# Performance work log

Measured on AMD Instinct MI355X. Metric: run time of the kernel, lower is better.

## Reference

```python
import jax, jax.numpy as jnp
import numpy as np

B, C_IN, H, W = 2, 256, 64, 64
D, NH, WS = 128, 8, 8          # embed_dim, num_heads, window_size
N_PTS = 8192
CAP = 256                      # max tokens per window (64 pixels + points, padded)
ODE_STEPS = 4                  # fixed-step RK4 approximating dopri5 on t in [0,1]


def setup_inputs() -> dict:
    key = jax.random.key(0)
    ks = jax.random.split(key, 16)
    p = lambda k, shape, fan: (jax.random.normal(k, shape, jnp.float32) / np.float32(np.sqrt(fan)))
    return {
        "in_image_feat": jax.random.normal(ks[0], (B, C_IN, H, W), jnp.float32),
        "pts_uv": jax.random.randint(ks[1], (N_PTS, 3), 0, 64),
        "pts_feat": jax.random.normal(ks[2], (N_PTS, D), jnp.float32),
        "conv_in_w": p(ks[3], (D, C_IN), C_IN),         # conv256_128 (1x1)
        "conv_in_b": jnp.zeros((D,), jnp.float32),
        "qkv_w": p(ks[4], (3 * D, D), D),               # sptr attn qkv
        "qkv_b": jnp.zeros((3 * D,), jnp.float32),
        "attnproj_w": p(ks[5], (D, D), D),              # sptr attn out proj
        "attnproj_b": jnp.zeros((D,), jnp.float32),
        "ode_w": p(ks[6], (D, D), D),                   # outimagefc128_128_ode
        "ode_b": jnp.zeros((D,), jnp.float32),
        "conv_out_w": p(ks[7], (C_IN, D), D),           # conv128_256 (1x1)
        "conv_out_b": jnp.zeros((C_IN,), jnp.float32),
    }


def _windowed_attention(feat, wid, NW, qkv_w, qkv_b, proj_w, proj_b):
    """Var-length windowed MHSA (sptr.VarLengthMultiheadSA) via pad-to-CAP."""
    T, d = feat.shape
    hd = d // NH
    order = jnp.argsort(wid)                      # stable sort by window id
    wid_s, feat_s = wid[order], feat[order]
    counts = jax.ops.segment_sum(jnp.ones_like(wid), wid, num_segments=NW)
    starts = jnp.cumsum(counts) - counts
    rank = jnp.arange(T) - starts[wid_s]          # within-window position
    valid = rank < CAP
    wid_w = jnp.where(valid, wid_s, NW)           # overflow -> dummy window
    rank_w = jnp.where(valid, rank, 0)
    buf = jnp.zeros((NW + 1, CAP, d), feat.dtype).at[wid_w, rank_w].set(feat_s)
    msk = jnp.zeros((NW + 1, CAP), bool).at[wid_w, rank_w].set(valid)
    qkv = buf @ qkv_w.T + qkv_b                   # [NW+1, CAP, 3d]
    q, k, v = (t.reshape(NW + 1, CAP, NH, hd) for t in jnp.split(qkv, 3, axis=-1))
    scores = jnp.einsum('wqhd,wkhd->whqk', q, k) / np.float32(np.sqrt(hd))
    scores = jnp.where(msk[:, None, None, :], scores, jnp.float32(-1e9))
    attn = jax.nn.softmax(scores, axis=-1)
    o = jnp.einsum('whqk,wkhd->wqhd', attn, v).reshape(NW + 1, CAP, d)
    o = o @ proj_w.T + proj_b
    out_s = jnp.where(valid[:, None], o[wid_w, rank_w], feat_s)
    return jnp.zeros_like(out_s).at[order].set(out_s)  # unsort


def reference(in_image_feat, pts_uv, pts_feat, conv_in_w, conv_in_b,
              qkv_w, qkv_b, attnproj_w, attnproj_b,
              ode_w, ode_b, conv_out_w, conv_out_b):
    b, c, h, w = in_image_feat.shape
    d = conv_in_w.shape[0]
    # 1x1 conv 256->128
    x = jnp.einsum('bchw,ec->bhwe', in_image_feat, conv_in_w) + conv_in_b
    pix_feat = x.reshape(b * h * w, d)
    # pixel uv grid (convert_image_to_uv): flatten order (b, h, w); u=w idx, v=h idx
    vv, uu = jnp.meshgrid(jnp.arange(h), jnp.arange(w), indexing='ij')
    pix_b = jnp.repeat(jnp.arange(b), h * w)
    pix_u = jnp.tile(uu.reshape(-1), b)
    pix_v = jnp.tile(vv.reshape(-1), b)
    # projected point uv (convert_pts_to_uv result, made in-range)
    pts_b = pts_uv[:, 0] % b
    pts_u = pts_uv[:, 1] % w
    pts_v = pts_uv[:, 2] % h
    tok_b = jnp.concatenate([pix_b, pts_b])
    tok_u = jnp.concatenate([pix_u, pts_u])
    tok_v = jnp.concatenate([pix_v, pts_v])
    feat = jnp.concatenate([pix_feat, pts_feat], axis=0)
    nwx, nwy = w // WS, h // WS
    wid = (tok_b * nwy + tok_v // WS) * nwx + tok_u // WS
    NW = b * nwx * nwy
    out = _windowed_attention(feat, wid, NW, qkv_w, qkv_b, attnproj_w, attnproj_b)
    img = out[: b * h * w]
    # fcode branch: odeint(ODEFunc(Linear), t=[0,1]) ~ fixed-step RK4, + residual
    f = lambda y: jax.nn.relu(y @ ode_w.T + ode_b)
    dt = jnp.float32(1.0 / ODE_STEPS)
    y = img
    for _ in range(ODE_STEPS):
        k1 = f(y); k2 = f(y + 0.5 * dt * k1); k3 = f(y + 0.5 * dt * k2); k4 = f(y + dt * k3)
        y = y + (dt / 6.0) * (k1 + 2.0 * k2 + 2.0 * k3 + k4)
    img = y + img
    # 1x1 conv 128->256 back to image layout
    img = img.reshape(b, h, w, d)
    return jnp.einsum('bhwd,cd->bchw', img, conv_out_w) + conv_out_b[None, :, None, None]
```

## Files before the change

### kernel.cpp

```cpp
#include <hip/hip_runtime.h>

typedef short bf16x8 __attribute__((ext_vector_type(8)));
typedef float f32x4 __attribute__((ext_vector_type(4)));

__device__ __forceinline__ float b2f(unsigned short s) {
    union { float f; unsigned u; } x; x.u = ((unsigned)s) << 16; return x.f;
}
__device__ __forceinline__ unsigned short f2b(float f) {
    unsigned u = __float_as_uint(f);
    unsigned r = (u + 0x7fffu + ((u >> 16) & 1u)) >> 16;
    return (unsigned short)r;
}

__global__ __launch_bounds__(256) void cast_k(const float* __restrict__ ciw,
                                              const float* __restrict__ qw,
                                              const float* __restrict__ pw,
                                              const float* __restrict__ ow,
                                              const float* __restrict__ cw,
                                              unsigned short* __restrict__ dst,
                                              int* __restrict__ cnt) {
    if (blockIdx.x == 0 && threadIdx.x < 128) cnt[threadIdx.x] = 0;
    int i = blockIdx.x * 256 + threadIdx.x;
    float v;
    if (i < 32768)        v = ciw[i];
    else if (i < 81920)   v = qw[i - 32768];
    else if (i < 98304)   v = pw[i - 81920];
    else if (i < 114688)  v = ow[i - 98304];
    else                  v = cw[i - 114688];
    dst[i] = f2b(v);
}

__global__ __launch_bounds__(256) void assign_k(const int* __restrict__ uv,
                                                int* __restrict__ cnt,
                                                int* __restrict__ wpts) {
    int i = blockIdx.x * 256 + threadIdx.x;
    if (i >= 8192) return;
    int b = uv[3 * i] & 1;
    int u = uv[3 * i + 1] & 63;
    int v = uv[3 * i + 2] & 63;
    int w = b * 64 + ((v >> 3) << 3) + (u >> 3);
    int slot = atomicAdd(cnt + w, 1);
    if (slot < 192) wpts[w * 192 + slot] = i;
}

__global__ __launch_bounds__(256) void cin_k(const float* __restrict__ in,
                                             const unsigned short* __restrict__ Wm,
                                             const float* __restrict__ bias,
                                             unsigned short* __restrict__ feat) {
    __shared__ unsigned short t[64][65];
    __shared__ unsigned short At[64][264];
    int p0 = blockIdx.x * 64, b = p0 >> 12, hw0 = p0 & 4095;
    int lane = threadIdx.x & 63, quad = threadIdx.x >> 6;
    for (int j = 0; j < 4; ++j) {
        int c0 = j * 64;
#pragma unroll
        for (int i = 0; i < 16; ++i) {
            int c = quad + i * 4;
            t[c][lane] = f2b(in[((size_t)(b * 256 + c0 + c)) * 4096 + hw0 + lane]);
        }
        __syncthreads();
#pragma unroll
        for (int i = 0; i < 16; ++i) {
            int p = quad + i * 4;
            At[p][c0 + lane] = t[lane][p];
        }
        __syncthreads();
    }
    int q = lane & 15, g = lane >> 4;
    int m0 = quad * 16;
    f32x4 acc[8];
#pragma unroll
    for (int tn = 0; tn < 8; ++tn) acc[tn] = (f32x4){0.f, 0.f, 0.f, 0.f};
#pragma unroll
    for (int k0 = 0; k0 < 256; k0 += 32) {
        bf16x8 a = *(const bf16x8*)&At[m0 + q][k0 + g * 8];
#pragma unroll
        for (int tn = 0; tn < 8; ++tn) {
            bf16x8 bfr = *(const bf16x8*)(Wm + (size_t)(tn * 16 + q) * 256 + k0 + g * 8);
            acc[tn] = __builtin_amdgcn_mfma_f32_16x16x32_bf16(a, bfr, acc[tn], 0, 0, 0);
        }
    }
#pragma unroll
    for (int tn = 0; tn < 8; ++tn) {
        int n = tn * 16 + q;
        float bs = bias[n];
#pragma unroll
        for (int rr = 0; rr < 4; ++rr)
            feat[(size_t)(p0 + m0 + g * 4 + rr) * 128 + n] = f2b(acc[tn][rr] + bs);
    }
}

__global__ __launch_bounds__(256) void qkv_k(const unsigned short* __restrict__ feat,
                                             const float* __restrict__ ptsf,
                                             const unsigned short* __restrict__ Wm,
                                             const float* __restrict__ bias,
                                             unsigned short* __restrict__ qkv) {
    if (blockIdx.x >= 128 && blockIdx.y < 2) return;
    int lane = threadIdx.x & 63, wv = threadIdx.x >> 6;
    int m0 = (blockIdx.x * 4 + wv) * 16;
    int q = lane & 15, g = lane >> 4;
    int nb = blockIdx.y * 64, koff = g * 8;
    bool isPt = m0 >= 8192;
    f32x4 acc[4];
#pragma unroll
    for (int tt = 0; tt < 4; ++tt) acc[tt] = (f32x4){0.f, 0.f, 0.f, 0.f};
#pragma unroll
    for (int k0 = 0; k0 < 128; k0 += 32) {
        bf16x8 a;
        if (isPt) {
            const float* pr = ptsf + (size_t)(m0 + q - 8192) * 128 + k0 + koff;
            float4 f0 = *(const float4*)pr;
            float4 f1 = *(const float4*)(pr + 4);
            a[0] = (short)f2b(f0.x); a[1] = (short)f2b(f0.y);
            a[2] = (short)f2b(f0.z); a[3] = (short)f2b(f0.w);
            a[4] = (short)f2b(f1.x); a[5] = (short)f2b(f1.y);
            a[6] = (short)f2b(f1.z); a[7] = (short)f2b(f1.w);
        } else {
            a = *(const bf16x8*)(feat + (size_t)(m0 + q) * 128 + k0 + koff);
        }
#pragma unroll
        for (int tt = 0; tt < 4; ++tt) {
            bf16x8 bfr = *(const bf16x8*)(Wm + (size_t)(nb + tt * 16 + q) * 128 + k0 + koff);
            acc[tt] = __builtin_amdgcn_mfma_f32_16x16x32_bf16(a, bfr, acc[tt], 0, 0, 0);
        }
    }
#pragma unroll
    for (int tt = 0; tt < 4; ++tt) {
        int n = nb + tt * 16 + q;
        float bs = bias[n];
#pragma unroll
        for (int rr = 0; rr < 4; ++rr)
            qkv[(size_t)(m0 + g * 4 + rr) * 384 + n] = f2b(acc[tt][rr] + bs);
    }
}

__global__ __launch_bounds__(256) void attn_k(const unsigned short* __restrict__ qkv,
                                              const int* __restrict__ cnt,
                                              const int* __restrict__ wpts,
                                              unsigned short* __restrict__ aout) {
    __shared__ unsigned short Kl[256][24];
    __shared__ unsigned short Vt[16][264];
    int blk = blockIdx.x;
    int w = blk >> 3, h = blk & 7;
    int b = w >> 6, wy = (w >> 3) & 7, wx = w & 7;
    int tid = threadIdx.x, wave = tid >> 6, lane = tid & 63;
    int q = lane & 15, g = lane >> 4;
    int c = cnt[w]; if (c > 192) c = 192;
    int T = 64 + c;
    {
        int t = tid;
        if (t < T) {
            int tok;
            if (t < 64) tok = b * 4096 + (wy * 8 + (t >> 3)) * 64 + wx * 8 + (t & 7);
            else        tok = 8192 + wpts[w * 192 + t - 64];
            const unsigned short* base = qkv + (size_t)tok * 384 + h * 16;
            bf16x8 k0 = *(const bf16x8*)(base + 128);
            bf16x8 v0 = *(const bf16x8*)(base + 256);
            *(bf16x8*)&Kl[t][0] = k0;
#pragma unroll
            for (int d = 0; d < 8; ++d) Vt[d][t] = (unsigned short)v0[d];
            bf16x8 k1 = *(const bf16x8*)(base + 136);
            bf16x8 v1 = *(const bf16x8*)(base + 264);
            *(bf16x8*)&Kl[t][8] = k1;
#pragma unroll
            for (int d = 0; d < 8; ++d) Vt[8 + d][t] = (unsigned short)v1[d];
        } else {
            bf16x8 z;
#pragma unroll
            for (int d = 0; d < 8; ++d) z[d] = 0;
            *(bf16x8*)&Kl[t][0] = z;
            *(bf16x8*)&Kl[t][8] = z;
#pragma unroll
            for (int d = 0; d < 16; ++d) Vt[d][t] = 0;
        }
    }
    int qq = wave * 16 + q;
    int qrow = b * 4096 + (wy * 8 + (qq >> 3)) * 64 + wx * 8 + (qq & 7);
    bf16x8 qfrag;
#pragma unroll
    for (int j = 0; j < 8; ++j) qfrag[j] = 0;
    if (g < 2) qfrag = *(const bf16x8*)(qkv + (size_t)qrow * 384 + h * 16 + g * 8);

    __syncthreads();

    float p[16][4];
    int MT = (T + 15) >> 4;
#pragma unroll
    for (int mt = 0; mt < 16; ++mt) {
        if (mt < MT) {
            bf16x8 af = *(const bf16x8*)&Kl[mt * 16 + q][(g & 1) * 8];
            f32x4 cc = (f32x4){0.f, 0.f, 0.f, 0.f};
            cc = __builtin_amdgcn_mfma_f32_16x16x32_bf16(af, qfrag, cc, 0, 0, 0);
#pragma unroll
            for (int r = 0; r < 4; ++r) {
                int tok = mt * 16 + g * 4 + r;
                p[mt][r] = (tok < T) ? cc[r] * 0.25f : -1e30f;
            }
        } else {
#pragma unroll
            for (int r = 0; r < 4; ++r) p[mt][r] = -1e30f;
        }
    }
    float mv = -3.0e38f;
#pragma unroll
    for (int mt = 0; mt < 16; ++mt)
#pragma unroll
        for (int r = 0; r < 4; ++r) mv = fmaxf(mv, p[mt][r]);
    mv = fmaxf(mv, __shfl_xor(mv, 16));
    mv = fmaxf(mv, __shfl_xor(mv, 32));
    float ls = 0.f;
#pragma unroll
    for (int mt = 0; mt < 16; ++mt)
#pragma unroll
        for (int r = 0; r < 4; ++r) {
            float e = __expf(p[mt][r] - mv);
            p[mt][r] = e;
            ls += e;
        }
    ls += __shfl_xor(ls, 16);
    ls += __shfl_xor(ls, 32);

    f32x4 oacc = (f32x4){0.f, 0.f, 0.f, 0.f};
    int KS = (T + 31) >> 5;
    int srcA = q + (((2 * g) & 3) << 4);
    int srcB = q + (((2 * g + 1) & 3) << 4);
#pragma unroll
    for (int ks = 0; ks < 8; ++ks) {
        if (ks < KS) {
            int n0lo, n0hi, n1lo, n1hi;
            asm("v_cvt_pk_bf16_f32 %0, %1, %2" : "=v"(n0lo) : "v"(p[2 * ks][0]), "v"(p[2 * ks][1]));
            asm("v_cvt_pk_bf16_f32 %0, %1, %2" : "=v"(n0hi) : "v"(p[2 * ks][2]), "v"(p[2 * ks][3]));
            asm("v_cvt_pk_bf16_f32 %0, %1, %2" : "=v"(n1lo) : "v"(p[2 * ks + 1][0]), "v"(p[2 * ks + 1][1]));
            asm("v_cvt_pk_bf16_f32 %0, %1, %2" : "=v"(n1hi) : "v"(p[2 * ks + 1][2]), "v"(p[2 * ks + 1][3]));
            int a0 = __shfl(n0lo, srcA), b0 = __shfl(n1lo, srcA);
            int a1 = __shfl(n0hi, srcA), b1 = __shfl(n1hi, srcA);
            int a2 = __shfl(n0lo, srcB), b2 = __shfl(n1lo, srcB);
            int a3 = __shfl(n0hi, srcB), b3 = __shfl(n1hi, srcB);
            union { int d[4]; bf16x8 v; } pb;
            bool lo2 = (g < 2);
            pb.d[0] = lo2 ? a0 : b0;
            pb.d[1] = lo2 ? a1 : b1;
            pb.d[2] = lo2 ? a2 : b2;
            pb.d[3] = lo2 ? a3 : b3;
            bf16x8 vf = *(const bf16x8*)&Vt[q][ks * 32 + g * 8];
            oacc = __builtin_amdgcn_mfma_f32_16x16x32_bf16(vf, pb.v, oacc, 0, 0, 0);
        }
    }
    float inv = 1.0f / ls;
    ushort4 st;
    st.x = f2b(oacc[0] * inv);
    st.y = f2b(oacc[1] * inv);
    st.z = f2b(oacc[2] * inv);
    st.w = f2b(oacc[3] * inv);
    *(ushort4*)(aout + (size_t)qrow * 128 + h * 16 + g * 4) = st;
}

__global__ __launch_bounds__(128) void tail_k(const unsigned short* __restrict__ aout,
                                              const unsigned short* __restrict__ pwb,
                                              const float* __restrict__ pb,
                                              const unsigned short* __restrict__ owb,
                                              const float* __restrict__ ob,
                                              const unsigned short* __restrict__ cwb,
                                              const float* __restrict__ cb,
                                              float* __restrict__ outp) {
    __shared__ unsigned short Wl[128][136];
    __shared__ unsigned short tc[2][16][136];
    int tid = threadIdx.x, wave = tid >> 6, lane = tid & 63;
    int g = lane >> 4, q = lane & 15;
    {
        int part = tid & 15;
#pragma unroll
        for (int it = 0; it < 16; ++it) {
            int rr = (tid >> 4) + it * 8;
            *(bf16x8*)&Wl[rr][part * 8] = *(const bf16x8*)(owb + rr * 128 + part * 8);
        }
    }
    int R0 = blockIdx.x * 16;
    int tnb = wave * 4;

    float y0[16];
    {
        const unsigned short* Arow = aout + (size_t)(R0 + q) * 128;
        f32x4 pacc[4];
#pragma unroll
        for (int t4 = 0; t4 < 4; ++t4) pacc[t4] = (f32x4){0.f, 0.f, 0.f, 0.f};
#pragma unroll
        for (int k0 = 0; k0 < 128; k0 += 32) {
            bf16x8 a = *(const bf16x8*)(Arow + k0 + g * 8);
#pragma unroll
            for (int t4 = 0; t4 < 4; ++t4) {
                bf16x8 bfr = *(const bf16x8*)(pwb + (size_t)((tnb + t4) * 16 + q) * 128 + k0 + g * 8);
                pacc[t4] = __builtin_amdgcn_mfma_f32_16x16x32_bf16(a, bfr, pacc[t4], 0, 0, 0);
            }
        }
#pragma unroll
        for (int t4 = 0; t4 < 4; ++t4) {
            float bsv = pb[(tnb + t4) * 16 + q];
#pragma unroll
            for (int rr = 0; rr < 4; ++rr) y0[t4 * 4 + rr] = pacc[t4][rr] + bsv;
        }
    }

    float bs[4];
#pragma unroll
    for (int t4 = 0; t4 < 4; ++t4) bs[t4] = ob[(tnb + t4) * 16 + q];
    float y[16], ac[16], ko[16];
#pragma unroll
    for (int i = 0; i < 16; ++i) y[i] = y0[i];

#define WRITE_TC(BUF, EXPR)                                               \
    {                                                                     \
        _Pragma("unroll")                                                 \
        for (int t4 = 0; t4 < 4; ++t4) {                                  \
            _Pragma("unroll")                                             \
            for (int rr = 0; rr < 4; ++rr) {                              \
                int i_ = t4 * 4 + rr;                                     \
                tc[BUF][g * 4 + rr][(tnb + t4) * 16 + q] = f2b(EXPR);     \
            }                                                             \
        }                                                                 \
        __syncthreads();                                                  \
    }

#define EVAL(BUF)                                                                      \
    {                                                                                  \
        bf16x8 af[4];                                                                  \
        _Pragma("unroll")                                                              \
        for (int tk = 0; tk < 4; ++tk)                                                 \
            af[tk] = *(const bf16x8*)&tc[BUF][q][tk * 32 + g * 8];                     \
        _Pragma("unroll")                                                              \
        for (int t4 = 0; t4 < 4; ++t4) {                                               \
            f32x4 cc = (f32x4){0.f, 0.f, 0.f, 0.f};                                    \
            _Pragma("unroll")                                                          \
            for (int tk = 0; tk < 4; ++tk) {                                           \
                bf16x8 bfr = *(const bf16x8*)&Wl[(tnb + t4) * 16 + q][tk * 32 + g * 8];\
                cc = __builtin_amdgcn_mfma_f32_16x16x32_bf16(af[tk], bfr, cc, 0, 0, 0);\
            }                                                                          \
            _Pragma("unroll")                                                          \
            for (int rr = 0; rr < 4; ++rr)                                             \
                ko[t4 * 4 + rr] = fmaxf(cc[rr] + bs[t4], 0.f);                         \
        }                                                                              \
    }

    WRITE_TC(0, y[i_])
    const float dt = 0.25f;
    for (int st = 0; st < 4; ++st) {
        EVAL(0);
#pragma unroll
        for (int i = 0; i < 16; ++i) ac[i] = y[i] + (dt / 6.f) * ko[i];
        WRITE_TC(1, y[i_] + (0.5f * dt) * ko[i_])
        EVAL(1);
#pragma unroll
        for (int i = 0; i < 16; ++i) ac[i] += (dt / 3.f) * ko[i];
        WRITE_TC(0, y[i_] + (0.5f * dt) * ko[i_])
        EVAL(0);
#pragma unroll
        for (int i = 0; i < 16; ++i) ac[i] += (dt / 3.f) * ko[i];
        WRITE_TC(1, y[i_] + dt * ko[i_])
        EVAL(1);
#pragma unroll
        for (int i = 0; i < 16; ++i) y[i] = ac[i] + (dt / 6.f) * ko[i];
        WRITE_TC(0, y[i_])
    }

    WRITE_TC(1, y[i_] + y0[i_])
    {
        int p = R0 + g * 4;
        int bb = p >> 12, plo = p & 4095;
#pragma unroll
        for (int t2 = 0; t2 < 8; ++t2) {
            int tn2 = wave * 8 + t2;
            f32x4 cc = (f32x4){0.f, 0.f, 0.f, 0.f};
#pragma unroll
            for (int tk = 0; tk < 4; ++tk) {
                bf16x8 af = *(const bf16x8*)&tc[1][q][tk * 32 + g * 8];
                bf16x8 bfr = *(const bf16x8*)(cwb + (size_t)(tn2 * 16 + q) * 128 + tk * 32 + g * 8);
                cc = __builtin_amdgcn_mfma_f32_16x16x32_bf16(af, bfr, cc, 0, 0, 0);
            }
            int ch = tn2 * 16 + q;
            float bsv = cb[ch];
            float4 stv;
            stv.x = cc[0] + bsv;
            stv.y = cc[1] + bsv;
            stv.z = cc[2] + bsv;
            stv.w = cc[3] + bsv;
            *(float4*)(outp + ((size_t)(bb * 256 + ch)) * 4096 + plo) = stv;
        }
    }
#undef WRITE_TC
#undef EVAL
}

extern "C" void kernel_launch(void* const* d_in, const int* in_sizes, int n_in,
                              void* d_out, int out_size, void* d_ws, size_t ws_size,
                              hipStream_t stream) {
    (void)in_sizes; (void)n_in; (void)out_size; (void)ws_size;
    const float* img_in = (const float*)d_in[0];
    const int*   pts_uv = (const int*)d_in[1];
    const float* ptsf   = (const float*)d_in[2];
    const float* ciw    = (const float*)d_in[3];
    const float* cib    = (const float*)d_in[4];
    const float* qw     = (const float*)d_in[5];
    const float* qb     = (const float*)d_in[6];
    const float* pw     = (const float*)d_in[7];
    const float* pb     = (const float*)d_in[8];
    const float* ow     = (const float*)d_in[9];
    const float* ob     = (const float*)d_in[10];
    const float* cw     = (const float*)d_in[11];
    const float* cb     = (const float*)d_in[12];

    char* ws = (char*)d_ws;
    unsigned short* feat = (unsigned short*)(ws);
    unsigned short* qkv  = (unsigned short*)(ws + 2097152);
    unsigned short* aout = (unsigned short*)(ws + 14680064);
    int*            cnt  = (int*)(ws + 16777216);
    int*            wpts = (int*)(ws + 16777728);
    unsigned short* wb   = (unsigned short*)(ws + 16876544);
    unsigned short* ciw_b = wb;
    unsigned short* qw_b  = wb + 32768;
    unsigned short* pw_b  = wb + 81920;
    unsigned short* ow_b  = wb + 98304;
    unsigned short* cw_b  = wb + 114688;

    cast_k<<<576, 256, 0, stream>>>(ciw, qw, pw, ow, cw, wb, cnt);
    assign_k<<<32, 256, 0, stream>>>(pts_uv, cnt, wpts);
    cin_k<<<128, 256, 0, stream>>>(img_in, ciw_b, cib, feat);
    qkv_k<<<dim3(256, 6), 256, 0, stream>>>(feat, ptsf, qw_b, qb, qkv);
    attn_k<<<1024, 256, 0, stream>>>(qkv, cnt, wpts, aout);
    tail_k<<<512, 128, 0, stream>>>(aout, pw_b, pb, ow_b, ob, cw_b, cb, (float*)d_out);
}
```

Measured before the change: 153.4 us.

## Fuse pixel input conv with QKV projection and split point QKV kernel

The 1x1 input convolution and the QKV projection for pixel tokens now run in one kernel. The conv result stays in shared memory, so the bf16 feature buffer no longer makes a round trip through global memory and one launch is removed. Point-token K/V projection moves to its own kernel that only computes columns 128-383, replacing the early-exit grid. The fused kernel uses small 128-thread blocks of 32 pixels each, which may lower occupancy, and its input transpose writes to shared memory with a strided pattern.

```diff
diff --git a/kernel.cpp b/kernel.cpp
--- a/kernel.cpp
+++ b/kernel.cpp
@@ -43,81 +43,93 @@
     if (slot < 192) wpts[w * 192 + slot] = i;
 }
 
-__global__ __launch_bounds__(256) void cin_k(const float* __restrict__ in,
-                                             const unsigned short* __restrict__ Wm,
-                                             const float* __restrict__ bias,
-                                             unsigned short* __restrict__ feat) {
-    __shared__ unsigned short t[64][65];
-    __shared__ unsigned short At[64][264];
-    int p0 = blockIdx.x * 64, b = p0 >> 12, hw0 = p0 & 4095;
-    int lane = threadIdx.x & 63, quad = threadIdx.x >> 6;
-    for (int j = 0; j < 4; ++j) {
-        int c0 = j * 64;
-#pragma unroll
-        for (int i = 0; i < 16; ++i) {
-            int c = quad + i * 4;
-            t[c][lane] = f2b(in[((size_t)(b * 256 + c0 + c)) * 4096 + hw0 + lane]);
-        }
-        __syncthreads();
-#pragma unroll
-        for (int i = 0; i < 16; ++i) {
-            int p = quad + i * 4;
-            At[p][c0 + lane] = t[lane][p];
-        }
-        __syncthreads();
-    }
+__global__ __launch_bounds__(128) void cinqkv_k(const float* __restrict__ in,
+                                                const unsigned short* __restrict__ ciwb,
+                                                const float* __restrict__ cib,
+                                                const unsigned short* __restrict__ qwb,
+                                                const float* __restrict__ qb,
+                                                unsigned short* __restrict__ qkv) {
+    __shared__ unsigned short At[32][264];
+    __shared__ unsigned short ft[32][136];
+    int p0 = blockIdx.x * 32, b = p0 >> 12, hw0 = p0 & 4095;
+    int tid = threadIdx.x, wave = tid >> 6, lane = tid & 63;
+    {
+        int px = tid & 31, chq = tid >> 5;
+#pragma unroll
+        for (int i = 0; i < 64; ++i) {
+            int c = chq + i * 4;
+            At[px][c] = f2b(in[((size_t)(b * 256 + c)) * 4096 + hw0 + px]);
+        }
+    }
+    __syncthreads();
     int q = lane & 15, g = lane >> 4;
-    int m0 = quad * 16;
-    f32x4 acc[8];
-#pragma unroll
-    for (int tn = 0; tn < 8; ++tn) acc[tn] = (f32x4){0.f, 0.f, 0.f, 0.f};
-#pragma unroll
-    for (int k0 = 0; k0 < 256; k0 += 32) {
-        bf16x8 a = *(const bf16x8*)&At[m0 + q][k0 + g * 8];
+    int m0 = wave * 16;
+    {
+        f32x4 acc[8];
+#pragma unroll
+        for (int tn = 0; tn < 8; ++tn) acc[tn] = (f32x4){0.f, 0.f, 0.f, 0.f};
+#pragma unroll
+        for (int k0 = 0; k0 < 256; k0 += 32) {
+            bf16x8 a = *(const bf16x8*)&At[m0 + q][k0 + g * 8];
+#pragma unroll
+            for (int tn = 0; tn < 8; ++tn) {
+                bf16x8 bfr = *(const bf16x8*)(ciwb + (size_t)(tn * 16 + q) * 256 + k0 + g * 8);
+                acc[tn] = __builtin_amdgcn_mfma_f32_16x16x32_bf16(a, bfr, acc[tn], 0, 0, 0);
+            }
+        }
 #pragma unroll
         for (int tn = 0; tn < 8; ++tn) {
-            bf16x8 bfr = *(const bf16x8*)(Wm + (size_t)(tn * 16 + q) * 256 + k0 + g * 8);
-            acc[tn] = __builtin_amdgcn_mfma_f32_16x16x32_bf16(a, bfr, acc[tn], 0, 0, 0);
-        }
-    }
-#pragma unroll
-    for (int tn = 0; tn < 8; ++tn) {
-        int n = tn * 16 + q;
-        float bs = bias[n];
-#pragma unroll
-        for (int rr = 0; rr < 4; ++rr)
-            feat[(size_t)(p0 + m0 + g * 4 + rr) * 128 + n] = f2b(acc[tn][rr] + bs);
-    }
-}
-
-__global__ __launch_bounds__(256) void qkv_k(const unsigned short* __restrict__ feat,
-                                             const float* __restrict__ ptsf,
-                                             const unsigned short* __restrict__ Wm,
-                                             const float* __restrict__ bias,
-                                             unsigned short* __restrict__ qkv) {
-    if (blockIdx.x >= 128 && blockIdx.y < 2) return;
+            int n = tn * 16 + q;
+            float bs = cib[n];
+#pragma unroll
+            for (int rr = 0; rr < 4; ++rr)
+                ft[m0 + g * 4 + rr][n] = f2b(acc[tn][rr] + bs);
+        }
+    }
+    __syncthreads();
+    {
+        bf16x8 af[4];
+#pragma unroll
+        for (int tk = 0; tk < 4; ++tk)
+            af[tk] = *(const bf16x8*)&ft[m0 + q][tk * 32 + g * 8];
+#pragma unroll
+        for (int tt = 0; tt < 24; ++tt) {
+            f32x4 cc = (f32x4){0.f, 0.f, 0.f, 0.f};
+#pragma unroll
+            for (int tk = 0; tk < 4; ++tk) {
+                bf16x8 bfr = *(const bf16x8*)(qwb + (size_t)(tt * 16 + q) * 128 + tk * 32 + g * 8);
+                cc = __builtin_amdgcn_mfma_f32_16x16x32_bf16(af[tk], bfr, cc, 0, 0, 0);
+            }
+            int n = tt * 16 + q;
+            float bsv = qb[n];
+#pragma unroll
+            for (int rr = 0; rr < 4; ++rr)
+                qkv[(size_t)(p0 + m0 + g * 4 + rr) * 384 + n] = f2b(cc[rr] + bsv);
+        }
+    }
+}
+
+__global__ __launch_bounds__(256) void ptqkv_k(const float* __restrict__ ptsf,
+                                               const unsigned short* __restrict__ Wm,
+                                               const float* __restrict__ bias,
+                                               unsigned short* __restrict__ qkv) {
     int lane = threadIdx.x & 63, wv = threadIdx.x >> 6;
-    int m0 = (blockIdx.x * 4 + wv) * 16;
+    int row = (blockIdx.x * 4 + wv) * 16;
     int q = lane & 15, g = lane >> 4;
-    int nb = blockIdx.y * 64, koff = g * 8;
-    bool isPt = m0 >= 8192;
+    int nb = 128 + blockIdx.y * 64, koff = g * 8;
     f32x4 acc[4];
 #pragma unroll
     for (int tt = 0; tt < 4; ++tt) acc[tt] = (f32x4){0.f, 0.f, 0.f, 0.f};
 #pragma unroll
     for (int k0 = 0; k0 < 128; k0 += 32) {
+        const float* pr = ptsf + (size_t)(row + q) * 128 + k0 + koff;
+        float4 f0 = *(const float4*)pr;
+        float4 f1 = *(const float4*)(pr + 4);
         bf16x8 a;
-        if (isPt) {
-            const float* pr = ptsf + (size_t)(m0 + q - 8192) * 128 + k0 + koff;
-            float4 f0 = *(const float4*)pr;
-            float4 f1 = *(const float4*)(pr + 4);
-            a[0] = (short)f2b(f0.x); a[1] = (short)f2b(f0.y);
-            a[2] = (short)f2b(f0.z); a[3] = (short)f2b(f0.w);
-            a[4] = (short)f2b(f1.x); a[5] = (short)f2b(f1.y);
-            a[6] = (short)f2b(f1.z); a[7] = (short)f2b(f1.w);
-        } else {
-            a = *(const bf16x8*)(feat + (size_t)(m0 + q) * 128 + k0 + koff);
-        }
+        a[0] = (short)f2b(f0.x); a[1] = (short)f2b(f0.y);
+        a[2] = (short)f2b(f0.z); a[3] = (short)f2b(f0.w);
+        a[4] = (short)f2b(f1.x); a[5] = (short)f2b(f1.y);
+        a[6] = (short)f2b(f1.z); a[7] = (short)f2b(f1.w);
 #pragma unroll
         for (int tt = 0; tt < 4; ++tt) {
             bf16x8 bfr = *(const bf16x8*)(Wm + (size_t)(nb + tt * 16 + q) * 128 + k0 + koff);
@@ -130,7 +142,7 @@
         float bs = bias[n];
 #pragma unroll
         for (int rr = 0; rr < 4; ++rr)
-            qkv[(size_t)(m0 + g * 4 + rr) * 384 + n] = f2b(acc[tt][rr] + bs);
+            qkv[(size_t)(8192 + row + g * 4 + rr) * 384 + n] = f2b(acc[tt][rr] + bs);
     }
 }
 
@@ -409,7 +421,6 @@
     const float* cb     = (const float*)d_in[12];
 
     char* ws = (char*)d_ws;
-    unsigned short* feat = (unsigned short*)(ws);
     unsigned short* qkv  = (unsigned short*)(ws + 2097152);
     unsigned short* aout = (unsigned short*)(ws + 14680064);
     int*            cnt  = (int*)(ws + 16777216);
@@ -423,8 +434,8 @@
 
     cast_k<<<576, 256, 0, stream>>>(ciw, qw, pw, ow, cw, wb, cnt);
     assign_k<<<32, 256, 0, stream>>>(pts_uv, cnt, wpts);
-    cin_k<<<128, 256, 0, stream>>>(img_in, ciw_b, cib, feat);
-    qkv_k<<<dim3(256, 6), 256, 0, stream>>>(feat, ptsf, qw_b, qb, qkv);
+    cinqkv_k<<<256, 128, 0, stream>>>(img_in, ciw_b, cib, qw_b, qb, qkv);
+    ptqkv_k<<<dim3(128, 4), 256, 0, stream>>>(ptsf, qw_b, qb, qkv);
     attn_k<<<1024, 256, 0, stream>>>(qkv, cnt, wpts, aout);
     tail_k<<<512, 128, 0, stream>>>(aout, pw_b, pb, ow_b, ob, cw_b, cb, (float*)d_out);
 }
```

After: 148.5 us. 1.03x faster.
